# Kernel optimization log

Measured on AMD Instinct MI355X. Metric: run time of the kernel, lower is better.

The kernel has to match this reference:

```python
import jax, jax.numpy as jnp
import numpy as np
import math

DIM = 96
D_MODEL = 2 * DIM
EXPAND = 2
D_INNER = EXPAND * D_MODEL  # 384
D_STATE = 16
D_CONV = 3
DT_RANK = math.ceil(D_MODEL / 16)  # 12
K = 4
B, H, W = 2, 56, 56


def setup_inputs() -> dict:
    key = jax.random.key(0)
    ks = jax.random.split(key, 10)
    s = lambda k, shp, sc=0.02: jax.random.normal(k, shp, jnp.float32) * sc
    inp = {}
    inp["x"] = jax.random.normal(ks[0], (B, DIM, H, W), jnp.float32)
    inp["conv_init_w"] = s(ks[1], (2 * DIM, DIM))
    inp["conv_init_b"] = jnp.zeros((2 * DIM,), jnp.float32)
    inp["in_proj_w"] = s(ks[2], (2 * D_INNER, D_MODEL))
    inp["conv2d_w"] = s(ks[3], (D_INNER, 1, D_CONV, D_CONV), 0.1)
    inp["conv2d_b"] = jnp.zeros((D_INNER,), jnp.float32)
    inp["x_proj_w"] = s(ks[4], (K, DT_RANK + 2 * D_STATE, D_INNER))
    inp["dt_proj_w"] = s(ks[5], (K, D_INNER, DT_RANK), 0.1)
    inp["dt_proj_b"] = s(ks[6], (K, D_INNER), 0.1)
    A = jnp.tile(jnp.arange(1, D_STATE + 1, dtype=jnp.float32), (K, D_INNER, 1))
    inp["A_log"] = jnp.log(A)  # (K, d_inner, d_state)
    inp["Ds"] = jnp.ones((K, D_INNER), jnp.float32)
    inp["ln_g"] = jnp.ones((D_INNER,), jnp.float32)
    inp["ln_b"] = jnp.zeros((D_INNER,), jnp.float32)
    inp["out_proj_w"] = s(ks[7], (D_MODEL, D_INNER))
    inp["conv_fina_w"] = s(ks[8], (DIM, 2 * DIM))
    inp["conv_fina_b"] = jnp.zeros((DIM,), jnp.float32)
    return inp


def _gelu(x):
    return jax.nn.gelu(x, approximate=False)


def _silu(x):
    return x * jax.nn.sigmoid(x)


def _selective_scan(u, delta, A, Bs, Cs, D):
    # u, delta: (b,K,d,L); A: (K,d,N); Bs,Cs: (b,K,N,L); D: (K,d)
    b, k, d, L = u.shape
    N = A.shape[-1]

    def step(hst, inp):
        u_t, dl_t, B_t, C_t = inp  # (b,K,d),(b,K,d),(b,K,N),(b,K,N)
        hst = jnp.exp(dl_t[..., None] * A) * hst + (dl_t * u_t)[..., None] * B_t[:, :, None, :]
        y = jnp.einsum('bkdn,bkn->bkd', hst, C_t)
        return hst, y

    seq = (jnp.moveaxis(u, -1, 0), jnp.moveaxis(delta, -1, 0),
           jnp.moveaxis(Bs, -1, 0), jnp.moveaxis(Cs, -1, 0))
    h0 = jnp.zeros((b, k, d, N), u.dtype)
    _, ys = jax.lax.scan(step, h0, seq)
    y = jnp.moveaxis(ys, 0, -1)  # (b,K,d,L)
    return y + u * D[None, :, :, None]


def reference(x, conv_init_w, conv_init_b, in_proj_w, conv2d_w, conv2d_b,
              x_proj_w, dt_proj_w, dt_proj_b, A_log, Ds, ln_g, ln_b,
              out_proj_w, conv_fina_w, conv_fina_b):
    b, c, h, w = x.shape
    # conv_init: 1x1 conv + GELU (dim -> 2*dim)
    x1 = _gelu(jnp.einsum('bchw,oc->bohw', x, conv_init_w) + conv_init_b[None, :, None, None])
    x0 = x1
    xh = jnp.transpose(x1, (0, 2, 3, 1))  # b h w c
    # --- SS2D ---
    xz = xh @ in_proj_w.T  # (b,h,w,2*d_inner)
    xi, z = jnp.split(xz, 2, axis=-1)
    xi = jnp.transpose(xi, (0, 3, 1, 2))  # b d h w
    xi = jax.lax.conv_general_dilated(xi, conv2d_w, (1, 1), 'SAME',
                                      dimension_numbers=('NCHW', 'OIHW', 'NCHW'),
                                      feature_group_count=xi.shape[1])
    xi = _silu(xi + conv2d_b[None, :, None, None])
    d = xi.shape[1]
    L = h * w
    x_flat = xi.reshape(b, d, L)
    x_tr = jnp.transpose(xi, (0, 1, 3, 2)).reshape(b, d, L)  # column-major scan
    xs = jnp.stack([x_flat, x_tr], axis=1)                   # (b,2,d,L)
    xs = jnp.concatenate([xs, jnp.flip(xs, axis=-1)], 1)     # (b,4,d,L)
    x_dbl = jnp.einsum('bkdl,kcd->bkcl', xs, x_proj_w)
    dts = x_dbl[:, :, :DT_RANK]
    Bs = x_dbl[:, :, DT_RANK:DT_RANK + D_STATE]
    Cs = x_dbl[:, :, DT_RANK + D_STATE:]
    dts = jnp.einsum('bkrl,kdr->bkdl', dts, dt_proj_w)
    delta = jax.nn.softplus(dts + dt_proj_b[None, :, :, None])
    A = -jnp.exp(A_log)  # (K,d,N)
    out_y = _selective_scan(xs, delta, A, Bs, Cs, Ds)  # (b,4,d,L)
    inv_y = jnp.flip(out_y[:, 2:4], axis=-1)
    y1 = out_y[:, 0]
    y2 = inv_y[:, 0]
    wb = lambda t: jnp.transpose(t.reshape(b, d, w, h), (0, 1, 3, 2)).reshape(b, d, L)
    y3 = wb(out_y[:, 1])
    y4 = wb(inv_y[:, 1])
    y = y1 + y2 + y3 + y4  # (b,d,L)
    y = jnp.transpose(y, (0, 2, 1)).reshape(b, h, w, d)
    mu = y.mean(-1, keepdims=True)
    var = ((y - mu) ** 2).mean(-1, keepdims=True)
    y = (y - mu) * jax.lax.rsqrt(var + 1e-5) * ln_g + ln_b
    y = y * _silu(z)
    y = y @ out_proj_w.T  # (b,h,w,d_model)
    y = jnp.transpose(y, (0, 3, 1, 2))  # b c h w
    # residual add with x0, then conv_fina 1x1 + GELU
    out = _gelu(jnp.einsum('bchw,oc->bohw', y + x0, conv_fina_w) + conv_fina_b[None, :, None, None])
    return out
```

## Files before the change

kernel.cpp:

```cpp
#include <hip/hip_runtime.h>


#define LPIX 3136
#define HH 56
#define SEG 49
#define SEGLEN 64
#define LOG2E 1.44269504f

__device__ __forceinline__ float gelu_f(float x) {
    return 0.5f * x * (1.0f + erff(x * 0.70710678118654752f));
}

__device__ __forceinline__ float quad_sum(float p) {
    p += __int_as_float(__builtin_amdgcn_update_dpp(0, __float_as_int(p), 0xB1, 0xf, 0xf, true));
    p += __int_as_float(__builtin_amdgcn_update_dpp(0, __float_as_int(p), 0x4E, 0xf, 0xf, true));
    return p;
}

template <int AM, int EM>
__global__ __launch_bounds__(256) void gemm_k(
    const float* __restrict__ A, const float* __restrict__ A2,
    const float* __restrict__ W, const float* __restrict__ bias,
    float* __restrict__ out0, int M, int N, int Kd)
{
    __shared__ __align__(16) float As[32][68];
    __shared__ __align__(16) float Ws[32][68];
    const int tid = threadIdx.x;
    const int m0 = blockIdx.x * 64;
    const int n0 = blockIdx.y * 64;
    const int mi = tid >> 4, ni = tid & 15;
    const int bI = m0 / LPIX, l0 = m0 % LPIX;
    float acc[4][4] = {};

    for (int k0 = 0; k0 < Kd; k0 += 32) {
        if constexpr (AM == 1) {
            int kr = tid >> 3, ms = (tid & 7) * 8;
            const float* pa = A + ((size_t)(bI * 96 + k0 + kr)) * LPIX + l0 + ms;
            *(float4*)&As[kr][ms] = *(const float4*)pa;
            *(float4*)&As[kr][ms + 4] = *(const float4*)(pa + 4);
        } else {
            #pragma unroll
            for (int p = 0; p < 2; ++p) {
                int r = (tid >> 3) + p * 32;
                int kv = (tid & 7) * 4;
                float4 v = *(const float4*)(A + (size_t)(m0 + r) * Kd + k0 + kv);
                float4 w2 = *(const float4*)(A2 + (size_t)(m0 + r) * Kd + k0 + kv);
                v.x += w2.x; v.y += w2.y; v.z += w2.z; v.w += w2.w;
                As[kv + 0][r] = v.x; As[kv + 1][r] = v.y;
                As[kv + 2][r] = v.z; As[kv + 3][r] = v.w;
            }
        }
        #pragma unroll
        for (int p = 0; p < 2; ++p) {
            int r = (tid >> 3) + p * 32;
            int kv = (tid & 7) * 4;
            int n = n0 + r;
            float4 v = make_float4(0.f, 0.f, 0.f, 0.f);
            if (n < N) v = *(const float4*)(W + (size_t)n * Kd + k0 + kv);
            Ws[kv + 0][r] = v.x; Ws[kv + 1][r] = v.y;
            Ws[kv + 2][r] = v.z; Ws[kv + 3][r] = v.w;
        }
        __syncthreads();
        #pragma unroll
        for (int kk = 0; kk < 32; ++kk) {
            float4 a = *(const float4*)&As[kk][mi * 4];
            float4 b = *(const float4*)&Ws[kk][ni * 4];
            float av[4] = {a.x, a.y, a.z, a.w};
            float bv[4] = {b.x, b.y, b.z, b.w};
            #pragma unroll
            for (int i = 0; i < 4; ++i)
                #pragma unroll
                for (int j = 0; j < 4; ++j)
                    acc[i][j] = fmaf(av[i], bv[j], acc[i][j]);
        }
        __syncthreads();
    }

    #pragma unroll
    for (int i = 0; i < 4; ++i) {
        int m = m0 + mi * 4 + i;
        int l = l0 + mi * 4 + i;
        int o0 = n0 + ni * 4;
        if constexpr (EM == 3) {
            #pragma unroll
            for (int j = 0; j < 4; ++j) {
                int o = o0 + j;
                if (o < N)
                    out0[((size_t)(bI * 96 + o)) * LPIX + l] = gelu_f(acc[i][j] + bias[o]);
            }
        } else {
            float4 g;
            g.x = gelu_f(acc[i][0] + bias[o0 + 0]);
            g.y = gelu_f(acc[i][1] + bias[o0 + 1]);
            g.z = gelu_f(acc[i][2] + bias[o0 + 2]);
            g.w = gelu_f(acc[i][3] + bias[o0 + 3]);
            *(float4*)&out0[(size_t)m * N + o0] = g;
        }
        (void)m;
    }
}

template <int EM>
__global__ __launch_bounds__(256) void gemm128_k(
    const float* __restrict__ A, const float* __restrict__ A2,
    const float* __restrict__ W,
    float* __restrict__ out0, float* __restrict__ out1,
    int M, int N, int Kd)
{
    __shared__ __align__(16) float As[32][132];
    __shared__ __align__(16) float Ws[32][68];
    const int tid = threadIdx.x;
    const int m0 = blockIdx.x * 128;
    const int n0 = blockIdx.y * 64;
    const int kz = blockIdx.z;
    const int mi = tid >> 4, ni = tid & 15;
    const float* Ap = A;
    const float* Wp = W;
    if constexpr (EM == 2) {
        if (kz & 1) Ap = A2;
        Wp += (size_t)kz * 44 * Kd;
    }
    float acc[8][4] = {};

    for (int k0 = 0; k0 < Kd; k0 += 32) {
        #pragma unroll
        for (int p = 0; p < 4; ++p) {
            int r = (tid >> 3) + p * 32;
            int kv = (tid & 7) * 4;
            float4 v = *(const float4*)(Ap + (size_t)(m0 + r) * Kd + k0 + kv);
            As[kv + 0][r] = v.x; As[kv + 1][r] = v.y;
            As[kv + 2][r] = v.z; As[kv + 3][r] = v.w;
        }
        #pragma unroll
        for (int p = 0; p < 2; ++p) {
            int r = (tid >> 3) + p * 32;
            int kv = (tid & 7) * 4;
            int n = n0 + r;
            float4 v = make_float4(0.f, 0.f, 0.f, 0.f);
            if (n < N) v = *(const float4*)(Wp + (size_t)n * Kd + k0 + kv);
            Ws[kv + 0][r] = v.x; Ws[kv + 1][r] = v.y;
            Ws[kv + 2][r] = v.z; Ws[kv + 3][r] = v.w;
        }
        __syncthreads();
        #pragma unroll
        for (int kk = 0; kk < 32; ++kk) {
            float4 a0 = *(const float4*)&As[kk][mi * 8];
            float4 a1 = *(const float4*)&As[kk][mi * 8 + 4];
            float4 b  = *(const float4*)&Ws[kk][ni * 4];
            float av[8] = {a0.x, a0.y, a0.z, a0.w, a1.x, a1.y, a1.z, a1.w};
            float bv[4] = {b.x, b.y, b.z, b.w};
            #pragma unroll
            for (int i = 0; i < 8; ++i)
                #pragma unroll
                for (int j = 0; j < 4; ++j)
                    acc[i][j] = fmaf(av[i], bv[j], acc[i][j]);
        }
        __syncthreads();
    }

    #pragma unroll
    for (int i = 0; i < 8; ++i) {
        int m = m0 + mi * 8 + i;
        int o0 = n0 + ni * 4;
        if constexpr (EM == 0) {
            *(float4*)&out0[(size_t)m * N + o0] =
                make_float4(acc[i][0], acc[i][1], acc[i][2], acc[i][3]);
        } else if constexpr (EM == 1) {
            float4 v = make_float4(acc[i][0], acc[i][1], acc[i][2], acc[i][3]);
            if (o0 < 384) *(float4*)&out0[(size_t)m * 384 + o0] = v;
            else          *(float4*)&out1[(size_t)m * 384 + (o0 - 384)] = v;
        } else {
            int bI = m / LPIX, l = m - bI * LPIX;
            #pragma unroll
            for (int j = 0; j < 4; ++j) {
                int o = o0 + j;
                if (o < 44)
                    out0[(((size_t)bI * 4 + kz) * LPIX + l) * 48 + o] = acc[i][j];
            }
        }
    }
}

__global__ __launch_bounds__(256) void dwsilu_k(
    const float* __restrict__ xs, const float* __restrict__ w9,
    const float* __restrict__ cb, const float* __restrict__ Ds,
    float* __restrict__ xiR, float* __restrict__ xiT, float* __restrict__ y0)
{
    __shared__ float S[32][339];
    const int h0 = blockIdx.x * 4;
    const int d0 = blockIdx.y * 32;
    const int b  = blockIdx.z;
    const int tid = threadIdx.x;
    const int fbase = h0 * HH - HH;
    if (tid < 32) { S[tid][0] = 0.f; S[tid][337] = 0.f; S[tid][338] = 0.f; }
    for (int it = tid; it < 336 * 8; it += 256) {
        int cc = it >> 3, q = it & 7;
        int f = fbase + cc;
        float4 v = make_float4(0.f, 0.f, 0.f, 0.f);
        if ((unsigned)f < LPIX)
            v = *(const float4*)(xs + ((size_t)b * LPIX + f) * 384 + d0 + q * 4);
        S[q * 4 + 0][cc + 1] = v.x; S[q * 4 + 1][cc + 1] = v.y;
        S[q * 4 + 2][cc + 1] = v.z; S[q * 4 + 3][cc + 1] = v.w;
    }
    __syncthreads();
    const int dl = tid & 31, fc = tid >> 5;
    const int d = d0 + dl;
    float wr[9];
    #pragma unroll
    for (int t = 0; t < 9; ++t) wr[t] = w9[d * 9 + t];
    const float bs = cb[d];
    const float sD = Ds[d] + Ds[384 + d] + Ds[768 + d] + Ds[1152 + d];
    const int hh = h0 + (fc >> 1);
    const int w0 = (fc & 1) * 28;
    for (int j = 0; j < 28; ++j) {
        int fl = fc * 28 + j;
        int f = h0 * HH + fl;
        int c = fl + 57;
        int w = w0 + j;
        float ml = (w > 0) ? 1.f : 0.f;
        float mr = (w < 55) ? 1.f : 0.f;
        float s = bs;
        #pragma unroll
        for (int tr = 0; tr < 3; ++tr) {
            int cc = c + (tr - 1) * 56;
            s = fmaf(S[dl][cc - 1], wr[tr * 3 + 0] * ml, s);
            s = fmaf(S[dl][cc],     wr[tr * 3 + 1], s);
            s = fmaf(S[dl][cc + 1], wr[tr * 3 + 2] * mr, s);
        }
        float v = s / (1.f + __expf(-s));
        size_t o = ((size_t)b * LPIX + f) * 384 + d;
        xiR[o] = v;
        y0[o] = v * sD;
        xiT[((size_t)b * LPIX + (w * HH + hh)) * 384 + d] = v;
    }
}

__global__ __launch_bounds__(256) void dtgemm_k(
    const float* __restrict__ xdblT, const float* __restrict__ dtw,
    const float* __restrict__ dtb, float* __restrict__ dT)
{
    __shared__ float As[64][13];
    __shared__ float Ws[64][13];
    int t0 = blockIdx.x * 64, d0 = blockIdx.y * 64;
    int bk = blockIdx.z, k = bk & 3;
    int tid = threadIdx.x;
    const float* Ab = xdblT + ((size_t)bk * LPIX + t0) * 48;
    for (int i = tid; i < 768; i += 256) {
        int tt = i / 12, r = i % 12;
        As[tt][r] = Ab[(size_t)tt * 48 + r];
    }
    for (int i = tid; i < 768; i += 256) {
        int dd = i / 12, r = i % 12;
        Ws[dd][r] = dtw[((size_t)k * 384 + d0 + dd) * 12 + r];
    }
    __syncthreads();
    int mi = tid >> 4, ni = tid & 15;
    float acc[4][4] = {};
    #pragma unroll
    for (int r = 0; r < 12; ++r) {
        float av[4], bv[4];
        #pragma unroll
        for (int i = 0; i < 4; ++i) av[i] = As[mi * 4 + i][r];
        #pragma unroll
        for (int j = 0; j < 4; ++j) bv[j] = Ws[ni * 4 + j][r];
        #pragma unroll
        for (int i = 0; i < 4; ++i)
            #pragma unroll
            for (int j = 0; j < 4; ++j)
                acc[i][j] = fmaf(av[i], bv[j], acc[i][j]);
    }
    #pragma unroll
    for (int i = 0; i < 4; ++i) {
        int t = t0 + mi * 4 + i;
        #pragma unroll
        for (int j = 0; j < 4; ++j) {
            int d = d0 + ni * 4 + j;
            float s = acc[i][j] + dtb[k * 384 + d];
            s = (s > 20.f) ? s : log1pf(__expf(s));
            dT[((size_t)bk * LPIX + t) * 384 + d] = s;
        }
    }
}

__global__ __launch_bounds__(256) void scan1_k(
    const float* __restrict__ dT, const float* __restrict__ xiR,
    const float* __restrict__ xiT, const float* __restrict__ xdblT,
    const float* __restrict__ A_log, float* __restrict__ lh,
    float* __restrict__ sumd)
{
    int w = blockIdx.x * 4 + (threadIdx.x >> 6);
    int lane = threadIdx.x & 63;
    int dl_ = lane >> 2, nq = lane & 3;
    int seg = w % SEG;
    int chain = w / SEG;
    int dblk = chain % 24;
    int bk = chain / 24;
    int b = bk >> 2, k = bk & 3;
    int d = dblk * 16 + dl_;

    float4 Ar = *reinterpret_cast<const float4*>(A_log + ((size_t)(k * 384 + d)) * 16 + nq * 4);
    float A2[4] = { -__expf(Ar.x) * LOG2E, -__expf(Ar.y) * LOG2E,
                    -__expf(Ar.z) * LOG2E, -__expf(Ar.w) * LOG2E };

    const float* pD = dT + (size_t)bk * LPIX * 384;
    const float* pU = ((k & 1) ? xiT : xiR) + (size_t)b * LPIX * 384;
    const float* pBC = xdblT + (size_t)bk * LPIX * 48;

    int t0 = seg * SEGLEN;
    int rev = k >> 1;
    int fpos0 = rev ? (LPIX - 1 - t0) : t0;
    int stepd = rev ? -384 : 384;
    int stepbc = rev ? -48 : 48;

    unsigned idx = (unsigned)fpos0 * 384u + (unsigned)d;
    unsigned ibc = (unsigned)fpos0 * 48u + 12u + (unsigned)nq * 4u;

    float h0 = 0.f, h1 = 0.f, h2 = 0.f, h3 = 0.f, sd = 0.f;

    float dlv = pD[idx], uv = pU[idx];
    float4 Bv = *reinterpret_cast<const float4*>(pBC + ibc);
    for (int s = 0; s < SEGLEN; ++s) {
        float dln, un; float4 Bn;
        if (s < SEGLEN - 1) {
            idx += stepd; ibc += stepbc;
            dln = pD[idx]; un = pU[idx];
            Bn = *reinterpret_cast<const float4*>(pBC + ibc);
        }
        sd += dlv;
        float dlu = dlv * uv;
        h0 = fmaf(__builtin_amdgcn_exp2f(dlv * A2[0]), h0, dlu * Bv.x);
        h1 = fmaf(__builtin_amdgcn_exp2f(dlv * A2[1]), h1, dlu * Bv.y);
        h2 = fmaf(__builtin_amdgcn_exp2f(dlv * A2[2]), h2, dlu * Bv.z);
        h3 = fmaf(__builtin_amdgcn_exp2f(dlv * A2[3]), h3, dlu * Bv.w);
        dlv = dln; uv = un; Bv = Bn;
    }
    size_t hb = (((size_t)seg * 8 + bk) * 384 + d) * 16 + nq * 4;
    *reinterpret_cast<float4*>(lh + hb) = make_float4(h0, h1, h2, h3);
    if (nq == 0)
        sumd[((size_t)seg * 8 + bk) * 384 + d] = sd;
}

__global__ __launch_bounds__(256) void scan2_k(
    float* __restrict__ lh, const float* __restrict__ sumd,
    const float* __restrict__ A_log)
{
    int idx = blockIdx.x * 256 + threadIdx.x;
    int n = idx & 15;
    int d = (idx >> 4) % 384;
    int bk = idx / (384 * 16);
    int k = bk & 3;
    float A2 = -__expf(A_log[((size_t)(k * 384 + d)) * 16 + n]) * LOG2E;
    float h = 0.f;
    for (int s = 0; s < SEG; ++s) {
        size_t base = (((size_t)s * 8 + bk) * 384 + d) * 16 + n;
        float lhv = lh[base];
        float P = __builtin_amdgcn_exp2f(sumd[((size_t)s * 8 + bk) * 384 + d] * A2);
        lh[base] = h;
        h = fmaf(P, h, lhv);
    }
}

template <int KK, int REV>
__device__ __forceinline__ void scan3_body(
    int b, int bk, int k, int seg, int d, int nq, int lane,
    const float* __restrict__ dT, const float* __restrict__ pU,
    const float* __restrict__ xdblT, const float* __restrict__ A_log,
    const float* __restrict__ lh, float* __restrict__ y0)
{
    float4 Ar = *reinterpret_cast<const float4*>(A_log + ((size_t)(k * 384 + d)) * 16 + nq * 4);
    float A2[4] = { -__expf(Ar.x) * LOG2E, -__expf(Ar.y) * LOG2E,
                    -__expf(Ar.z) * LOG2E, -__expf(Ar.w) * LOG2E };

    const float* pD = dT + (size_t)bk * LPIX * 384;
    const float* pBC = xdblT + (size_t)bk * LPIX * 48;
    float* pY = y0 + (size_t)b * LPIX * 384;

    int t0 = seg * SEGLEN;
    int fpos0 = REV ? (LPIX - 1 - t0) : t0;
    constexpr int stepd = REV ? -384 : 384;
    constexpr int stepbc = REV ? -48 : 48;

    unsigned idx = (unsigned)fpos0 * 384u + (unsigned)d;
    unsigned ibc = (unsigned)fpos0 * 48u + 12u + (unsigned)nq * 4u;

    unsigned iy; int rr;
    if constexpr (KK) {
        int r0 = fpos0 % 56, q0 = fpos0 / 56;
        rr = r0;
        iy = (unsigned)(r0 * 56 + q0) * 384u + (unsigned)d;
    } else {
        iy = idx;
        rr = 0; (void)rr;
    }

    size_t hb = (((size_t)seg * 8 + bk) * 384 + d) * 16 + nq * 4;
    float4 h4 = *reinterpret_cast<const float4*>(lh + hb);
    float h0 = h4.x, h1 = h4.y, h2 = h4.z, h3 = h4.w;

    float dlv = pD[idx], uv = pU[idx];
    float4 Bv = *reinterpret_cast<const float4*>(pBC + ibc);
    float4 Cv = *reinterpret_cast<const float4*>(pBC + ibc + 16);

    for (int s = 0; s < SEGLEN; ++s) {
        float dln, un; float4 Bn, Cn;
        if (s < SEGLEN - 1) {
            idx += stepd; ibc += stepbc;
            dln = pD[idx]; un = pU[idx];
            Bn = *reinterpret_cast<const float4*>(pBC + ibc);
            Cn = *reinterpret_cast<const float4*>(pBC + ibc + 16);
        }
        float dlu = dlv * uv;
        h0 = fmaf(__builtin_amdgcn_exp2f(dlv * A2[0]), h0, dlu * Bv.x);
        float p = h0 * Cv.x;
        h1 = fmaf(__builtin_amdgcn_exp2f(dlv * A2[1]), h1, dlu * Bv.y);
        p = fmaf(h1, Cv.y, p);
        h2 = fmaf(__builtin_amdgcn_exp2f(dlv * A2[2]), h2, dlu * Bv.z);
        p = fmaf(h2, Cv.z, p);
        h3 = fmaf(__builtin_amdgcn_exp2f(dlv * A2[3]), h3, dlu * Bv.w);
        p = fmaf(h3, Cv.w, p);
        p = quad_sum(p);
        if ((lane & 3) == 0)
            __hip_atomic_fetch_add(pY + iy, p,
                                   __ATOMIC_RELAXED, __HIP_MEMORY_SCOPE_AGENT);
        if constexpr (KK) {
            if constexpr (REV) {
                bool wrap = (rr == 0);
                iy += wrap ? (unsigned)(3079 * 384) : (unsigned)(-56 * 384);
                rr = wrap ? 55 : rr - 1;
            } else {
                bool wrap = (rr == 55);
                iy += wrap ? (unsigned)(-3079 * 384) : (unsigned)(56 * 384);
                rr = wrap ? 0 : rr + 1;
            }
        } else {
            iy += (unsigned)stepd;
        }
        dlv = dln; uv = un; Bv = Bn; Cv = Cn;
    }
}

__global__ __launch_bounds__(256) void scan3_k(
    const float* __restrict__ dT, const float* __restrict__ xiR,
    const float* __restrict__ xiT, const float* __restrict__ xdblT,
    const float* __restrict__ A_log, const float* __restrict__ lh,
    float* __restrict__ y0)
{
    int w = blockIdx.x * 4 + (threadIdx.x >> 6);
    int lane = threadIdx.x & 63;
    int dl_ = lane >> 2, nq = lane & 3;
    int seg = w % SEG;
    int chain = w / SEG;
    int dblk = chain % 24;
    int bk = chain / 24;
    int b = bk >> 2, k = bk & 3;
    int d = dblk * 16 + dl_;
    const float* pU = ((k & 1) ? xiT : xiR) + (size_t)b * LPIX * 384;
    if (k == 0)      scan3_body<0, 0>(b, bk, k, seg, d, nq, lane, dT, pU, xdblT, A_log, lh, y0);
    else if (k == 1) scan3_body<1, 0>(b, bk, k, seg, d, nq, lane, dT, pU, xdblT, A_log, lh, y0);
    else if (k == 2) scan3_body<0, 1>(b, bk, k, seg, d, nq, lane, dT, pU, xdblT, A_log, lh, y0);
    else             scan3_body<1, 1>(b, bk, k, seg, d, nq, lane, dT, pU, xdblT, A_log, lh, y0);
}

__global__ __launch_bounds__(256) void lngate_k(
    const float* __restrict__ y0, const float* __restrict__ z,
    const float* __restrict__ lng, const float* __restrict__ lnb,
    float* __restrict__ gbuf)
{
    int m = blockIdx.x * 4 + (threadIdx.x >> 6);
    int lane = threadIdx.x & 63;
    const float* py = y0 + (size_t)m * 384;
    float v[6];
    float s = 0.f, sq = 0.f;
    #pragma unroll
    for (int i = 0; i < 6; ++i) {
        v[i] = py[lane + i * 64];
        s += v[i]; sq += v[i] * v[i];
    }
    #pragma unroll
    for (int off = 1; off < 64; off <<= 1) {
        s += __shfl_xor(s, off);
        sq += __shfl_xor(sq, off);
    }
    float mu = s * (1.f / 384.f);
    float var = sq * (1.f / 384.f) - mu * mu;
    float rs = rsqrtf(var + 1e-5f);
    const float* pz = z + (size_t)m * 384;
    float* pg = gbuf + (size_t)m * 384;
    #pragma unroll
    for (int i = 0; i < 6; ++i) {
        int ch = lane + i * 64;
        float nv = (v[i] - mu) * rs * lng[ch] + lnb[ch];
        float zv = pz[ch];
        pg[ch] = nv * (zv / (1.f + __expf(-zv)));
    }
}

extern "C" void kernel_launch(void* const* d_in, const int* in_sizes, int n_in,
                              void* d_out, int out_size, void* d_ws, size_t ws_size,
                              hipStream_t stream) {
    const float* x        = (const float*)d_in[0];
    const float* w_init   = (const float*)d_in[1];
    const float* b_init   = (const float*)d_in[2];
    const float* w_inproj = (const float*)d_in[3];
    const float* w_conv   = (const float*)d_in[4];
    const float* b_conv   = (const float*)d_in[5];
    const float* w_xproj  = (const float*)d_in[6];
    const float* w_dt     = (const float*)d_in[7];
    const float* b_dt     = (const float*)d_in[8];
    const float* A_log    = (const float*)d_in[9];
    const float* Ds       = (const float*)d_in[10];
    const float* ln_g     = (const float*)d_in[11];
    const float* ln_b     = (const float*)d_in[12];
    const float* w_out    = (const float*)d_in[13];
    const float* w_fina   = (const float*)d_in[14];
    const float* b_fina   = (const float*)d_in[15];

    float* ws    = (float*)d_ws;
    float* x1    = ws + 0;
    float* xis   = ws + 1204224;
    float* lh    = ws + 1204224;
    float* z     = ws + 3612672;
    float* xiR   = ws + 6021120;
    float* xiT   = ws + 8429568;
    float* xdblT = ws + 10838016;
    float* dT    = ws + 12042240;
    float* y0    = ws + 21676032;
    float* sumd  = ws + 24084480;
    float* out   = (float*)d_out;

    gemm_k<1, 4><<<dim3(98, 3), 256, 0, stream>>>(x, nullptr, w_init, b_init,
                                                  x1, 6272, 192, 96);
    gemm128_k<1><<<dim3(49, 12), 256, 0, stream>>>(x1, nullptr, w_inproj,
                                                   xis, z, 6272, 768, 192);
    dwsilu_k<<<dim3(14, 12, 2), 256, 0, stream>>>(xis, w_conv, b_conv, Ds,
                                                  xiR, xiT, y0);
    gemm128_k<2><<<dim3(49, 1, 4), 256, 0, stream>>>(xiR, xiT, w_xproj,
                                                     xdblT, nullptr, 6272, 44, 384);
    dtgemm_k<<<dim3(49, 6, 8), 256, 0, stream>>>(xdblT, w_dt, b_dt, dT);
    scan1_k<<<2352, 256, 0, stream>>>(dT, xiR, xiT, xdblT, A_log, lh, sumd);
    scan2_k<<<192, 256, 0, stream>>>(lh, sumd, A_log);
    scan3_k<<<2352, 256, 0, stream>>>(dT, xiR, xiT, xdblT, A_log, lh, y0);
    lngate_k<<<1568, 256, 0, stream>>>(y0, z, ln_g, ln_b, xiR);
    gemm128_k<0><<<dim3(49, 3), 256, 0, stream>>>(xiR, nullptr, w_out,
                                                  xiT, nullptr, 6272, 192, 384);
    gemm_k<2, 3><<<dim3(98, 2), 256, 0, stream>>>(xiT, x1, w_fina, b_fina,
                                                  out, 6272, 96, 192);
}
```

Baseline: 402.6 us.

## Emit local-scan outputs in pass one and add cheap carry-in correction pass

The first chunked-scan pass now also produces y from a zero initial state, atomically accumulating it, and overwrites dT in place with the running cumulative delta. The third pass no longer recomputes the recurrence. It adds the carry-in contribution C·exp(A·cumdelta)·h_in, which reads only cumdelta and C and skips segment 0. Segments change from 49×64 to 32×98, which reduces the carry-propagation work but lengthens each serial chain. The cost is extra atomics and dT writes in pass one, and dT is destroyed for any later consumer.

Result: slower. 422.6 us (+5.0%).

```diff
diff --git a/kernel.cpp b/kernel.cpp
--- a/kernel.cpp
+++ b/kernel.cpp
@@ -3,8 +3,8 @@
 
 #define LPIX 3136
 #define HH 56
-#define SEG 49
-#define SEGLEN 64
+#define SEG 32
+#define SEGLEN 98
 #define LOG2E 1.44269504f
 
 __device__ __forceinline__ float gelu_f(float x) {
@@ -282,11 +282,95 @@
     }
 }
 
-__global__ __launch_bounds__(256) void scan1_k(
-    const float* __restrict__ dT, const float* __restrict__ xiR,
+template <int KK, int REV>
+__device__ __forceinline__ void scan1y_body(
+    int b, int bk, int k, int seg, int d, int nq, int lane,
+    float* __restrict__ dT, const float* __restrict__ pU,
+    const float* __restrict__ xdblT, const float* __restrict__ A_log,
+    float* __restrict__ lh, float* __restrict__ sumd, float* __restrict__ y0)
+{
+    float4 Ar = *(const float4*)(A_log + ((size_t)(k * 384 + d)) * 16 + nq * 4);
+    float A2[4] = { -__expf(Ar.x) * LOG2E, -__expf(Ar.y) * LOG2E,
+                    -__expf(Ar.z) * LOG2E, -__expf(Ar.w) * LOG2E };
+
+    float* pD = dT + (size_t)bk * LPIX * 384;
+    const float* pBC = xdblT + (size_t)bk * LPIX * 48;
+    float* pY = y0 + (size_t)b * LPIX * 384;
+
+    int t0 = seg * SEGLEN;
+    int fpos0 = REV ? (LPIX - 1 - t0) : t0;
+    constexpr int stepd = REV ? -384 : 384;
+    constexpr int stepbc = REV ? -48 : 48;
+
+    unsigned idxL = (unsigned)fpos0 * 384u + (unsigned)d;
+    unsigned ibcL = (unsigned)fpos0 * 48u + 12u + (unsigned)nq * 4u;
+    unsigned idxC = idxL;
+
+    unsigned iy; int rr = 0;
+    if constexpr (KK) {
+        int r0 = fpos0 % 56, q0 = fpos0 / 56;
+        rr = r0;
+        iy = (unsigned)(r0 * 56 + q0) * 384u + (unsigned)d;
+    } else {
+        iy = idxL;
+    }
+
+    float h0 = 0.f, h1 = 0.f, h2 = 0.f, h3 = 0.f, sd = 0.f;
+    float dlv = pD[idxL], uv = pU[idxL];
+    float4 Bv = *(const float4*)(pBC + ibcL);
+    float4 Cv = *(const float4*)(pBC + ibcL + 16);
+    idxL += stepd; ibcL += stepbc;
+
+    for (int s = 0; s < SEGLEN; ++s) {
+        float dln, un; float4 Bn, Cn;
+        if (s < SEGLEN - 1) {
+            dln = pD[idxL]; un = pU[idxL];
+            Bn = *(const float4*)(pBC + ibcL);
+            Cn = *(const float4*)(pBC + ibcL + 16);
+            idxL += stepd; ibcL += stepbc;
+        }
+        sd += dlv;
+        if (nq == 0) pD[idxC] = sd;
+        float dlu = dlv * uv;
+        h0 = fmaf(__builtin_amdgcn_exp2f(dlv * A2[0]), h0, dlu * Bv.x);
+        float p = h0 * Cv.x;
+        h1 = fmaf(__builtin_amdgcn_exp2f(dlv * A2[1]), h1, dlu * Bv.y);
+        p = fmaf(h1, Cv.y, p);
+        h2 = fmaf(__builtin_amdgcn_exp2f(dlv * A2[2]), h2, dlu * Bv.z);
+        p = fmaf(h2, Cv.z, p);
+        h3 = fmaf(__builtin_amdgcn_exp2f(dlv * A2[3]), h3, dlu * Bv.w);
+        p = fmaf(h3, Cv.w, p);
+        p = quad_sum(p);
+        if ((lane & 3) == 0)
+            __hip_atomic_fetch_add(pY + iy, p,
+                                   __ATOMIC_RELAXED, __HIP_MEMORY_SCOPE_AGENT);
+        idxC += stepd;
+        if constexpr (KK) {
+            if constexpr (REV) {
+                bool wrap = (rr == 0);
+                iy += wrap ? (unsigned)(3079 * 384) : (unsigned)(-56 * 384);
+                rr = wrap ? 55 : rr - 1;
+            } else {
+                bool wrap = (rr == 55);
+                iy += wrap ? (unsigned)(-3079 * 384) : (unsigned)(56 * 384);
+                rr = wrap ? 0 : rr + 1;
+            }
+        } else {
+            iy += (unsigned)stepd;
+        }
+        dlv = dln; uv = un; Bv = Bn; Cv = Cn;
+    }
+    size_t hb = (((size_t)seg * 8 + bk) * 384 + d) * 16 + nq * 4;
+    *(float4*)(lh + hb) = make_float4(h0, h1, h2, h3);
+    if (nq == 0)
+        sumd[((size_t)seg * 8 + bk) * 384 + d] = sd;
+}
+
+__global__ __launch_bounds__(256) void scan1y_k(
+    float* __restrict__ dT, const float* __restrict__ xiR,
     const float* __restrict__ xiT, const float* __restrict__ xdblT,
     const float* __restrict__ A_log, float* __restrict__ lh,
-    float* __restrict__ sumd)
+    float* __restrict__ sumd, float* __restrict__ y0)
 {
     int w = blockIdx.x * 4 + (threadIdx.x >> 6);
     int lane = threadIdx.x & 63;
@@ -297,47 +381,11 @@
     int bk = chain / 24;
     int b = bk >> 2, k = bk & 3;
     int d = dblk * 16 + dl_;
-
-    float4 Ar = *reinterpret_cast<const float4*>(A_log + ((size_t)(k * 384 + d)) * 16 + nq * 4);
-    float A2[4] = { -__expf(Ar.x) * LOG2E, -__expf(Ar.y) * LOG2E,
-                    -__expf(Ar.z) * LOG2E, -__expf(Ar.w) * LOG2E };
-
-    const float* pD = dT + (size_t)bk * LPIX * 384;
     const float* pU = ((k & 1) ? xiT : xiR) + (size_t)b * LPIX * 384;
-    const float* pBC = xdblT + (size_t)bk * LPIX * 48;
-
-    int t0 = seg * SEGLEN;
-    int rev = k >> 1;
-    int fpos0 = rev ? (LPIX - 1 - t0) : t0;
-    int stepd = rev ? -384 : 384;
-    int stepbc = rev ? -48 : 48;
-
-    unsigned idx = (unsigned)fpos0 * 384u + (unsigned)d;
-    unsigned ibc = (unsigned)fpos0 * 48u + 12u + (unsigned)nq * 4u;
-
-    float h0 = 0.f, h1 = 0.f, h2 = 0.f, h3 = 0.f, sd = 0.f;
-
-    float dlv = pD[idx], uv = pU[idx];
-    float4 Bv = *reinterpret_cast<const float4*>(pBC + ibc);
-    for (int s = 0; s < SEGLEN; ++s) {
-        float dln, un; float4 Bn;
-        if (s < SEGLEN - 1) {
-            idx += stepd; ibc += stepbc;
-            dln = pD[idx]; un = pU[idx];
-            Bn = *reinterpret_cast<const float4*>(pBC + ibc);
-        }
-        sd += dlv;
-        float dlu = dlv * uv;
-        h0 = fmaf(__builtin_amdgcn_exp2f(dlv * A2[0]), h0, dlu * Bv.x);
-        h1 = fmaf(__builtin_amdgcn_exp2f(dlv * A2[1]), h1, dlu * Bv.y);
-        h2 = fmaf(__builtin_amdgcn_exp2f(dlv * A2[2]), h2, dlu * Bv.z);
-        h3 = fmaf(__builtin_amdgcn_exp2f(dlv * A2[3]), h3, dlu * Bv.w);
-        dlv = dln; uv = un; Bv = Bn;
-    }
-    size_t hb = (((size_t)seg * 8 + bk) * 384 + d) * 16 + nq * 4;
-    *reinterpret_cast<float4*>(lh + hb) = make_float4(h0, h1, h2, h3);
-    if (nq == 0)
-        sumd[((size_t)seg * 8 + bk) * 384 + d] = sd;
+    if (k == 0)      scan1y_body<0, 0>(b, bk, k, seg, d, nq, lane, dT, pU, xdblT, A_log, lh, sumd, y0);
+    else if (k == 1) scan1y_body<1, 0>(b, bk, k, seg, d, nq, lane, dT, pU, xdblT, A_log, lh, sumd, y0);
+    else if (k == 2) scan1y_body<0, 1>(b, bk, k, seg, d, nq, lane, dT, pU, xdblT, A_log, lh, sumd, y0);
+    else             scan1y_body<1, 1>(b, bk, k, seg, d, nq, lane, dT, pU, xdblT, A_log, lh, sumd, y0);
 }
 
 __global__ __launch_bounds__(256) void scan2_k(
@@ -361,15 +409,17 @@
 }
 
 template <int KK, int REV>
-__device__ __forceinline__ void scan3_body(
+__device__ __forceinline__ void corr_body(
     int b, int bk, int k, int seg, int d, int nq, int lane,
-    const float* __restrict__ dT, const float* __restrict__ pU,
-    const float* __restrict__ xdblT, const float* __restrict__ A_log,
-    const float* __restrict__ lh, float* __restrict__ y0)
-{
-    float4 Ar = *reinterpret_cast<const float4*>(A_log + ((size_t)(k * 384 + d)) * 16 + nq * 4);
+    const float* __restrict__ dT, const float* __restrict__ xdblT,
+    const float* __restrict__ A_log, const float* __restrict__ lh,
+    float* __restrict__ y0)
+{
+    float4 Ar = *(const float4*)(A_log + ((size_t)(k * 384 + d)) * 16 + nq * 4);
     float A2[4] = { -__expf(Ar.x) * LOG2E, -__expf(Ar.y) * LOG2E,
                     -__expf(Ar.z) * LOG2E, -__expf(Ar.w) * LOG2E };
+    size_t hb = (((size_t)seg * 8 + bk) * 384 + d) * 16 + nq * 4;
+    float4 hin = *(const float4*)(lh + hb);
 
     const float* pD = dT + (size_t)bk * LPIX * 384;
     const float* pBC = xdblT + (size_t)bk * LPIX * 48;
@@ -381,47 +431,31 @@
     constexpr int stepbc = REV ? -48 : 48;
 
     unsigned idx = (unsigned)fpos0 * 384u + (unsigned)d;
-    unsigned ibc = (unsigned)fpos0 * 48u + 12u + (unsigned)nq * 4u;
-
-    unsigned iy; int rr;
+    unsigned ic = (unsigned)fpos0 * 48u + 28u + (unsigned)nq * 4u;
+
+    unsigned iy; int rr = 0;
     if constexpr (KK) {
         int r0 = fpos0 % 56, q0 = fpos0 / 56;
         rr = r0;
         iy = (unsigned)(r0 * 56 + q0) * 384u + (unsigned)d;
     } else {
         iy = idx;
-        rr = 0; (void)rr;
-    }
-
-    size_t hb = (((size_t)seg * 8 + bk) * 384 + d) * 16 + nq * 4;
-    float4 h4 = *reinterpret_cast<const float4*>(lh + hb);
-    float h0 = h4.x, h1 = h4.y, h2 = h4.z, h3 = h4.w;
-
-    float dlv = pD[idx], uv = pU[idx];
-    float4 Bv = *reinterpret_cast<const float4*>(pBC + ibc);
-    float4 Cv = *reinterpret_cast<const float4*>(pBC + ibc + 16);
-
+    }
+
+    #pragma unroll 2
     for (int s = 0; s < SEGLEN; ++s) {
-        float dln, un; float4 Bn, Cn;
-        if (s < SEGLEN - 1) {
-            idx += stepd; ibc += stepbc;
-            dln = pD[idx]; un = pU[idx];
-            Bn = *reinterpret_cast<const float4*>(pBC + ibc);
-            Cn = *reinterpret_cast<const float4*>(pBC + ibc + 16);
-        }
-        float dlu = dlv * uv;
-        h0 = fmaf(__builtin_amdgcn_exp2f(dlv * A2[0]), h0, dlu * Bv.x);
-        float p = h0 * Cv.x;
-        h1 = fmaf(__builtin_amdgcn_exp2f(dlv * A2[1]), h1, dlu * Bv.y);
-        p = fmaf(h1, Cv.y, p);
-        h2 = fmaf(__builtin_amdgcn_exp2f(dlv * A2[2]), h2, dlu * Bv.z);
-        p = fmaf(h2, Cv.z, p);
-        h3 = fmaf(__builtin_amdgcn_exp2f(dlv * A2[3]), h3, dlu * Bv.w);
-        p = fmaf(h3, Cv.w, p);
+        float cum = pD[idx];
+        float4 C = *(const float4*)(pBC + ic);
+        float p;
+        p =          C.x * (__builtin_amdgcn_exp2f(cum * A2[0]) * hin.x);
+        p = fmaf(C.y, __builtin_amdgcn_exp2f(cum * A2[1]) * hin.y, p);
+        p = fmaf(C.z, __builtin_amdgcn_exp2f(cum * A2[2]) * hin.z, p);
+        p = fmaf(C.w, __builtin_amdgcn_exp2f(cum * A2[3]) * hin.w, p);
         p = quad_sum(p);
         if ((lane & 3) == 0)
             __hip_atomic_fetch_add(pY + iy, p,
                                    __ATOMIC_RELAXED, __HIP_MEMORY_SCOPE_AGENT);
+        idx += stepd; ic += stepbc;
         if constexpr (KK) {
             if constexpr (REV) {
                 bool wrap = (rr == 0);
@@ -435,13 +469,11 @@
         } else {
             iy += (unsigned)stepd;
         }
-        dlv = dln; uv = un; Bv = Bn; Cv = Cn;
-    }
-}
-
-__global__ __launch_bounds__(256) void scan3_k(
-    const float* __restrict__ dT, const float* __restrict__ xiR,
-    const float* __restrict__ xiT, const float* __restrict__ xdblT,
+    }
+}
+
+__global__ __launch_bounds__(256) void corr_k(
+    const float* __restrict__ dT, const float* __restrict__ xdblT,
     const float* __restrict__ A_log, const float* __restrict__ lh,
     float* __restrict__ y0)
 {
@@ -449,16 +481,16 @@
     int lane = threadIdx.x & 63;
     int dl_ = lane >> 2, nq = lane & 3;
     int seg = w % SEG;
+    if (seg == 0) return;
     int chain = w / SEG;
     int dblk = chain % 24;
     int bk = chain / 24;
     int b = bk >> 2, k = bk & 3;
     int d = dblk * 16 + dl_;
-    const float* pU = ((k & 1) ? xiT : xiR) + (size_t)b * LPIX * 384;
-    if (k == 0)      scan3_body<0, 0>(b, bk, k, seg, d, nq, lane, dT, pU, xdblT, A_log, lh, y0);
-    else if (k == 1) scan3_body<1, 0>(b, bk, k, seg, d, nq, lane, dT, pU, xdblT, A_log, lh, y0);
-    else if (k == 2) scan3_body<0, 1>(b, bk, k, seg, d, nq, lane, dT, pU, xdblT, A_log, lh, y0);
-    else             scan3_body<1, 1>(b, bk, k, seg, d, nq, lane, dT, pU, xdblT, A_log, lh, y0);
+    if (k == 0)      corr_body<0, 0>(b, bk, k, seg, d, nq, lane, dT, xdblT, A_log, lh, y0);
+    else if (k == 1) corr_body<1, 0>(b, bk, k, seg, d, nq, lane, dT, xdblT, A_log, lh, y0);
+    else if (k == 2) corr_body<0, 1>(b, bk, k, seg, d, nq, lane, dT, xdblT, A_log, lh, y0);
+    else             corr_body<1, 1>(b, bk, k, seg, d, nq, lane, dT, xdblT, A_log, lh, y0);
 }
 
 __global__ __launch_bounds__(256) void lngate_k(
@@ -537,9 +569,9 @@
     gemm128_k<2><<<dim3(49, 1, 4), 256, 0, stream>>>(xiR, xiT, w_xproj,
                                                      xdblT, nullptr, 6272, 44, 384);
     dtgemm_k<<<dim3(49, 6, 8), 256, 0, stream>>>(xdblT, w_dt, b_dt, dT);
-    scan1_k<<<2352, 256, 0, stream>>>(dT, xiR, xiT, xdblT, A_log, lh, sumd);
+    scan1y_k<<<1536, 256, 0, stream>>>(dT, xiR, xiT, xdblT, A_log, lh, sumd, y0);
     scan2_k<<<192, 256, 0, stream>>>(lh, sumd, A_log);
-    scan3_k<<<2352, 256, 0, stream>>>(dT, xiR, xiT, xdblT, A_log, lh, y0);
+    corr_k<<<1536, 256, 0, stream>>>(dT, xdblT, A_log, lh, y0);
     lngate_k<<<1568, 256, 0, stream>>>(y0, z, ln_g, ln_b, xiR);
     gemm128_k<0><<<dim3(49, 3), 256, 0, stream>>>(xiR, nullptr, w_out,
                                                   xiT, nullptr, 6272, 192, 384);
```
